# Kernel tuning notes

Measured on AMD Instinct MI355X. Metric: run time of the kernel, lower is better.

Reference implementation:

```python
import jax, jax.numpy as jnp
import numpy as np


def setup_inputs() -> dict:
    key = jax.random.key(0)
    ks = jax.random.split(key, 4)
    B, D, H, W, C = 1, 24, 24, 24, 256
    C_ = C // 8
    x = jax.random.normal(ks[0], (B, D, H, W, C), dtype=jnp.float32)
    # 1x1x1 Conv3D kernels are just [C_in, C_out] matrices (glorot-ish scale)
    wg = jax.random.normal(ks[1], (C, C_), dtype=jnp.float32) * (1.0 / np.sqrt(C))
    wf = jax.random.normal(ks[2], (C, C_), dtype=jnp.float32) * (1.0 / np.sqrt(C))
    wh = jax.random.normal(ks[3], (C, C), dtype=jnp.float32) * (1.0 / np.sqrt(C))
    bg = jnp.zeros((C_,), dtype=jnp.float32)
    bf = jnp.zeros((C_,), dtype=jnp.float32)
    bh = jnp.zeros((C,), dtype=jnp.float32)
    gamma = jnp.zeros((C,), dtype=jnp.float32)  # module initializes gamma to zeros
    return {"x": x, "wg": wg, "bg": bg, "wf": wf, "bf": bf, "wh": wh, "bh": bh, "gamma": gamma}


def reference(x, wg, bg, wf, bf, wh, bh, gamma):
    B, D, H, W, C = x.shape
    N = D * H * W
    xt = x.reshape(B, N, C)                      # [B, N, C] tokens
    x_g = jnp.einsum('bnc,cf->bnf', xt, wg) + bg  # [B, N, C_] (query)
    x_f = jnp.einsum('bnc,cf->bnf', xt, wf) + bf  # [B, N, C_] (key)
    x_h = jnp.einsum('bnc,cd->bnd', xt, wh) + bh  # [B, N, C]  (value)
    s = jnp.einsum('bnf,bmf->bnm', x_g, x_f)      # [B, N, N] scores
    s = jax.nn.softmax(s, axis=-1)
    o = jnp.einsum('bnm,bmd->bnd', s, x_h)        # [B, N, C]
    o = o.reshape(B, D, H, W, C)
    return gamma * o + x
```

## Files before the change

### kernel.cpp

```cpp
#include <hip/hip_runtime.h>
#include <math.h>

#define N_TOK 13824
#define KT 64
#define LOG2E 1.44269504088896f
#define M0 40.0f

typedef __attribute__((ext_vector_type(8)))  short bf16x8;
typedef __attribute__((ext_vector_type(4)))  float f32x4;
typedef __attribute__((ext_vector_type(16))) float f32x16;
typedef __attribute__((ext_vector_type(8)))  unsigned short u16x8;
typedef unsigned short u16;

#define AS3(p) ((__attribute__((address_space(3))) void*)(p))
#define AS1(p) ((const __attribute__((address_space(1))) void*)(p))
#define GLL(gp, lp) __builtin_amdgcn_global_load_lds(AS1(gp), AS3(lp), 16, 0, 0)

__device__ inline u16 f2b(float v) {
    union { float f; unsigned u; } a; a.f = v;
    unsigned r = a.u + 0x7fffu + ((a.u >> 16) & 1u);
    return (u16)(r >> 16);
}
__device__ inline float b2f(u16 v) {
    union { unsigned u; float f; } a; a.u = ((unsigned)v) << 16; return a.f;
}
__device__ inline float dev_exp2(float x) {
    float r;
    asm volatile("v_exp_f32 %0, %1" : "=v"(r) : "v"(x));
    return r;
}
__device__ inline float cross_sum(float v) {
    float a = v, b = v;
    asm volatile("v_permlane32_swap_b32 %0, %1" : "+v"(a), "+v"(b));
    return a + b;
}
__device__ inline unsigned cvtpk(float lo, float hi) {
    unsigned r;
    asm volatile("v_cvt_pk_bf16_f32 %0, %1, %2" : "=v"(r) : "v"(lo), "v"(hi));
    return r;
}

__global__ __launch_bounds__(512) void prep_kernel(
    const float* __restrict__ wh, const float* __restrict__ wg,
    const float* __restrict__ wf, u16* __restrict__ wt)
{
    int id = blockIdx.x * 512 + threadIdx.x;
    if (id < 320 * 256) {
        int n = id >> 8, k = id & 255;
        float v = (n < 256) ? wh[k * 256 + n]
                : (n < 288) ? wg[k * 32 + (n - 256)] * LOG2E
                            : wf[k * 32 + (n - 288)];
        wt[n * 256 + k] = f2b(v);
    }
}

__global__ __launch_bounds__(256) void proj_kernel(
    const float* __restrict__ x, const u16* __restrict__ wt,
    const float* __restrict__ bg, const float* __restrict__ bfv, const float* __restrict__ bh,
    u16* __restrict__ g, u16* __restrict__ f, u16* __restrict__ ht)
{
    __shared__ float Asf[4096];
    __shared__ u16 Bs[64 * 64];
    const int t = threadIdx.x, l = t & 63, w = t >> 6;
    const int m0 = blockIdx.x * 64, n0 = blockIdx.y * 64;
    const int mh = (w & 1) * 32, nh = (w >> 1) * 32;
    f32x4 acc[2][2] = {};

    int aoff[4];
    #pragma unroll
    for (int i = 0; i < 4; ++i) {
        int p = i * 256 + t;
        int row = p >> 4, up = p & 15, uu = up ^ (row & 15);
        aoff[i] = row * 256 + uu * 4;
    }

    for (int kstep = 0; kstep < 4; ++kstep) {
        const int k0 = kstep * 64;
        __syncthreads();
        #pragma unroll
        for (int i = 0; i < 4; ++i)
            GLL(x + (size_t)m0 * 256 + k0 + aoff[i], Asf + (i * 256 + t) * 4);
        #pragma unroll
        for (int i = 0; i < 2; ++i) {
            int ch  = w * 2 + i;
            int row = ch * 8 + (l >> 3);
            int ul  = (l & 7) ^ ((l >> 3) & 7);
            GLL(wt + (size_t)(n0 + row) * 256 + k0 + ul * 8, Bs + ch * 512);
        }
        asm volatile("s_waitcnt vmcnt(0)" ::: "memory");
        __syncthreads();
        #pragma unroll
        for (int ks = 0; ks < 2; ++ks) {
            bf16x8 a[2], b[2];
            #pragma unroll
            for (int mf = 0; mf < 2; ++mf) {
                int row = mh + mf * 16 + (l & 15);
                int uu0 = ks * 8 + (l >> 4) * 2;
                f32x4 f0 = *(const f32x4*)&Asf[(row * 16 + (uu0 ^ (row & 15))) * 4];
                f32x4 f1 = *(const f32x4*)&Asf[(row * 16 + ((uu0 + 1) ^ (row & 15))) * 4];
                union { unsigned u[4]; bf16x8 v; } av;
                av.u[0] = cvtpk(f0[0], f0[1]);
                av.u[1] = cvtpk(f0[2], f0[3]);
                av.u[2] = cvtpk(f1[0], f1[1]);
                av.u[3] = cvtpk(f1[2], f1[3]);
                a[mf] = av.v;
            }
            #pragma unroll
            for (int nf = 0; nf < 2; ++nf) {
                int row = nh + nf * 16 + (l & 15);
                int u   = (ks * 4 + (l >> 4)) ^ (row & 7);
                b[nf] = *(const bf16x8*)(Bs + row * 64 + u * 8);
            }
            #pragma unroll
            for (int mf = 0; mf < 2; ++mf)
                #pragma unroll
                for (int nf = 0; nf < 2; ++nf)
                    acc[mf][nf] = __builtin_amdgcn_mfma_f32_16x16x32_bf16(
                        a[mf], b[nf], acc[mf][nf], 0, 0, 0);
        }
    }

    #pragma unroll
    for (int mf = 0; mf < 2; ++mf)
        #pragma unroll
        for (int nf = 0; nf < 2; ++nf) {
            const int row0 = m0 + mh + mf * 16 + (l >> 4) * 4;
            const int col  = n0 + nh + nf * 16 + (l & 15);
            if (col < 256) {
                const float bias = bh[col];
                ushort4 o;
                o.x = f2b(acc[mf][nf][0] + bias);
                o.y = f2b(acc[mf][nf][1] + bias);
                o.z = f2b(acc[mf][nf][2] + bias);
                o.w = f2b(acc[mf][nf][3] + bias);
                *(ushort4*)(ht + (size_t)col * N_TOK + row0) = o;
            } else {
                const float bias = (col < 288) ? bg[col - 256] * LOG2E : bfv[col - 288];
                #pragma unroll
                for (int r = 0; r < 4; ++r) {
                    u16 v = f2b(acc[mf][nf][r] + bias);
                    if (col < 288) g[(size_t)(row0 + r) * 32 + (col - 256)] = v;
                    else           f[(size_t)(row0 + r) * 32 + (col - 288)] = v;
                }
            }
        }
}

__global__ __launch_bounds__(256, 2) void attn_kernel(
    const u16* __restrict__ g, const u16* __restrict__ fk, const u16* __restrict__ ht,
    u16* __restrict__ po, float* __restrict__ pl,
    int kps, int ntiles, int nwg)
{
    __shared__ u16 VtF[2 * 16384];
    __shared__ u16 KsF[2 * 2048];

    int orig = blockIdx.x + blockIdx.y * 108;
    int qd = nwg >> 3, rr = nwg & 7;
    int xcd = orig & 7, idx = orig >> 3;
    int wgid = (xcd < rr ? xcd * (qd + 1) : rr * (qd + 1) + (xcd - rr) * qd) + idx;
    const int split = wgid / 108;
    const int qblk  = wgid % 108;

    const int t = threadIdx.x, l = t & 63, w = t >> 6;
    const int hi = l >> 5, l31 = l & 31;
    const int q0 = qblk * 128 + w * 32;
    const int kbase = split * kps;

    bf16x8 qf0 = *(const bf16x8*)(g + (size_t)(q0 + l31) * 32 + hi * 8);
    bf16x8 qf1 = *(const bf16x8*)(g + (size_t)(q0 + l31) * 32 + 16 + hi * 8);

    f32x16 acc[8] = {};
    float l_run = 0.f;

    const u16* vbase = ht + kbase;
    int voffV[8];
    #pragma unroll
    for (int i = 0; i < 8; ++i) {
        int u = i * 256 + t;
        int ch = u >> 3, gg = u & 7, kg = gg ^ (ch & 7);
        voffV[i] = ch * N_TOK + kg * 8;
    }
    int koffK;
    { int key = t >> 2, gcu = t & 3, cu = gcu ^ ((key >> 1) & 3);
      koffK = key * 32 + cu * 8; }
    const u16* kbp = fk + (size_t)kbase * 32;

    int rbV[4];
    #pragma unroll
    for (int i = 0; i < 4; ++i) {
        int kg = i * 2 + hi;
        rbV[i] = l31 * 64 + ((kg ^ (l31 & 7)) * 8);
    }
    int rbK[2];
    #pragma unroll
    for (int ks = 0; ks < 2; ++ks)
        rbK[ks] = l31 * 4 * 8 + (((ks * 2 + hi) ^ ((l31 >> 1) & 3)) * 8);

    auto stage = [&](int tile, int db) {
        const u16* vs = vbase + tile * KT;
        #pragma unroll
        for (int i = 0; i < 8; ++i)
            GLL(vs + voffV[i], &VtF[db * 16384 + (i * 256 + t) * 8]);
        GLL(kbp + tile * (KT * 32) + koffK, &KsF[db * 2048 + t * 8]);
    };

    stage(0, 0);

    auto pvblock = [&](int b, int kb, unsigned pa[2][4]) {
        #pragma unroll
        for (int ks = 0; ks < 2; ++ks) {
            union { unsigned u[4]; bf16x8 v; } pb;
            pb.u[0] = pa[ks][0]; pb.u[1] = pa[ks][1];
            pb.u[2] = pa[ks][2]; pb.u[3] = pa[ks][3];
            #pragma unroll
            for (int cht = 0; cht < 8; ++cht) {
                bf16x8 vf = *(const bf16x8*)&VtF[b * 16384 + cht * 2048 + rbV[kb * 2 + ks]];
                acc[cht] = __builtin_amdgcn_mfma_f32_32x32x16_bf16(
                    pb.v, vf, acc[cht], 0, 0, 0);
            }
        }
    };

    auto softpa = [&](const f32x16& s, unsigned pa[2][4]) -> float {
        float pv[16];
        #pragma unroll
        for (int r = 0; r < 16; ++r) pv[r] = dev_exp2(s[r] - M0);
        #pragma unroll
        for (int ks = 0; ks < 2; ++ks) {
            const int o = ks * 8;
            unsigned a0 = cvtpk(pv[o + 0], pv[o + 1]);
            unsigned b0 = cvtpk(pv[o + 2], pv[o + 3]);
            unsigned a1 = cvtpk(pv[o + 4], pv[o + 5]);
            unsigned b1 = cvtpk(pv[o + 6], pv[o + 7]);
            asm volatile("v_permlane32_swap_b32 %0, %1" : "+v"(a0), "+v"(a1));
            asm volatile("v_permlane32_swap_b32 %0, %1" : "+v"(b0), "+v"(b1));
            pa[ks][0] = a0; pa[ks][1] = b0;
            pa[ks][2] = a1; pa[ks][3] = b1;
        }
        float s8[8];
        #pragma unroll
        for (int i = 0; i < 8; ++i) s8[i] = pv[i] + pv[i + 8];
        float s4a = s8[0] + s8[1], s4b = s8[2] + s8[3];
        float s4c = s8[4] + s8[5], s4d = s8[6] + s8[7];
        return (s4a + s4b) + (s4c + s4d);
    };

    auto sub = [&](int b, int cur) {
        asm volatile("" ::: "memory");
        __builtin_amdgcn_s_barrier();
        asm volatile("" ::: "memory");
        { int nx = cur + 1 < ntiles ? cur + 1 : 0; stage(nx, b ^ 1); }
        asm volatile("s_waitcnt vmcnt(9)" ::: "memory");
        __builtin_amdgcn_s_barrier();
        asm volatile("" ::: "memory");

        bf16x8 kf[2][2];
        #pragma unroll
        for (int kb = 0; kb < 2; ++kb)
            #pragma unroll
            for (int ks = 0; ks < 2; ++ks)
                kf[kb][ks] = *(const bf16x8*)&KsF[b * 2048 + kb * 1024 + rbK[ks]];

        f32x16 s0, s1;
        {
            f32x16 zz = {};
            zz = __builtin_amdgcn_mfma_f32_32x32x16_bf16(kf[0][0], qf0, zz, 0, 0, 0);
            s0 = __builtin_amdgcn_mfma_f32_32x32x16_bf16(kf[0][1], qf1, zz, 0, 0, 0);
        }
        {
            f32x16 zz = {};
            zz = __builtin_amdgcn_mfma_f32_32x32x16_bf16(kf[1][0], qf0, zz, 0, 0, 0);
            s1 = __builtin_amdgcn_mfma_f32_32x32x16_bf16(kf[1][1], qf1, zz, 0, 0, 0);
        }

        unsigned pa0[2][4], pa1[2][4];
        float t0 = softpa(s0, pa0);
        pvblock(b, 0, pa0);
        float t1 = softpa(s1, pa1);
        pvblock(b, 1, pa1);
        l_run += t0 + t1;
    };

    for (int tl = 0; tl < ntiles; tl += 2) {
        sub(0, tl);
        sub(1, tl + 1);
    }

    #pragma unroll
    for (int cht = 0; cht < 8; ++cht) {
        int ch = cht * 32 + l31;
        #pragma unroll
        for (int r = 0; r < 16; ++r) {
            int qq = q0 + (r & 3) + 8 * (r >> 2) + 4 * hi;
            po[((size_t)split * N_TOK + qq) * 256 + ch] = f2b(acc[cht][r]);
        }
    }
    float lfull = cross_sum(l_run);
    if (hi == 0) {
        int qq = q0 + l31;
        pl[(size_t)split * N_TOK + qq] = lfull;
    }
}

__global__ __launch_bounds__(256) void combine_kernel(
    const u16* __restrict__ po, const float* __restrict__ pl,
    const float* __restrict__ x, const float* __restrict__ gamma, float* __restrict__ out,
    int nsplit)
{
    const int t = threadIdx.x;
    const int q = blockIdx.x * 8 + (t >> 5);
    const int c8 = (t & 31) * 8;

    float lsum = 0.f, o[8] = {};
    for (int s = 0; s < nsplit; ++s) {
        lsum += pl[(size_t)s * N_TOK + q];
        u16x8 p8 = *(const u16x8*)(po + ((size_t)s * N_TOK + q) * 256 + c8);
        #pragma unroll
        for (int j = 0; j < 8; ++j) o[j] += b2f(p8[j]);
    }
    float inv = 1.f / lsum;
    float4 gm0 = *(const float4*)(gamma + c8);
    float4 gm1 = *(const float4*)(gamma + c8 + 4);
    float4 xv0 = *(const float4*)(x + (size_t)q * 256 + c8);
    float4 xv1 = *(const float4*)(x + (size_t)q * 256 + c8 + 4);
    float4 ov0, ov1;
    ov0.x = gm0.x * (o[0] * inv) + xv0.x;
    ov0.y = gm0.y * (o[1] * inv) + xv0.y;
    ov0.z = gm0.z * (o[2] * inv) + xv0.z;
    ov0.w = gm0.w * (o[3] * inv) + xv0.w;
    ov1.x = gm1.x * (o[4] * inv) + xv1.x;
    ov1.y = gm1.y * (o[5] * inv) + xv1.y;
    ov1.z = gm1.z * (o[6] * inv) + xv1.z;
    ov1.w = gm1.w * (o[7] * inv) + xv1.w;
    *(float4*)(out + (size_t)q * 256 + c8)     = ov0;
    *(float4*)(out + (size_t)q * 256 + c8 + 4) = ov1;
}

extern "C" void kernel_launch(void* const* d_in, const int* in_sizes, int n_in,
                              void* d_out, int out_size, void* d_ws, size_t ws_size,
                              hipStream_t stream) {
    const float* x     = (const float*)d_in[0];
    const float* wg    = (const float*)d_in[1];
    const float* bg    = (const float*)d_in[2];
    const float* wf    = (const float*)d_in[3];
    const float* bfv   = (const float*)d_in[4];
    const float* wh    = (const float*)d_in[5];
    const float* bh    = (const float*)d_in[6];
    const float* gamma = (const float*)d_in[7];
    float* out = (float*)d_out;

    const size_t base_b = (size_t)N_TOK * 640;
    auto need = [&](int ns) {
        return base_b + (size_t)ns * N_TOK * 512 + (size_t)ns * N_TOK * 8
             + 320 * 256 * 2 + 1024;
    };
    int nsplit = 4;
    if (ws_size >= need(9)) nsplit = 9;
    else if (ws_size >= need(6)) nsplit = 6;
    const int kps = N_TOK / nsplit, ntiles = kps / KT;
    const int nwg = 108 * nsplit;

    u16* ws = (u16*)d_ws;
    u16* gq = ws;
    u16* fk = gq + (size_t)N_TOK * 32;
    u16* ht = fk + (size_t)N_TOK * 32;
    u16* po = ht + (size_t)N_TOK * 256;
    u16* wt = po + (size_t)nsplit * N_TOK * 256;
    float* pl = (float*)(wt + 320 * 256);

    prep_kernel<<<160, 512, 0, stream>>>(wh, wg, wf, wt);
    proj_kernel<<<dim3(216, 5), 256, 0, stream>>>(x, wt, bg, bfv, bh, gq, fk, ht);
    attn_kernel<<<dim3(108, nsplit), 256, 0, stream>>>(gq, fk, ht, po, pl, kps, ntiles, nwg);
    combine_kernel<<<N_TOK / 8, 256, 0, stream>>>(po, pl, x, gamma, out, nsplit);
}
```

Before: 143.6 us.

## Shrink attention workgroups to two waves with 32-key tiles and new LDS swizzle

The attention kernel now uses 128-thread workgroups, each covering 64 queries instead of 128, with key tiles of 32 instead of 64. The launch grid doubles to 216 blocks per split, and the LDS staging layout and swizzle are rewritten to match the smaller tiles. Each iteration now does one score block instead of two. The aim is more, smaller workgroups, which should fill the CUs better and cut per-block LDS use. The cost is that each loaded V/K tile is reused by fewer queries and there are twice as many barrier and stage rounds per key.

```diff
diff --git a/kernel.cpp b/kernel.cpp
--- a/kernel.cpp
+++ b/kernel.cpp
@@ -2,7 +2,7 @@
 #include <math.h>
 
 #define N_TOK 13824
-#define KT 64
+#define KT 32
 #define LOG2E 1.44269504088896f
 #define M0 40.0f
 
@@ -146,24 +146,24 @@
         }
 }
 
-__global__ __launch_bounds__(256, 2) void attn_kernel(
+__global__ __launch_bounds__(128, 2) void attn_kernel(
     const u16* __restrict__ g, const u16* __restrict__ fk, const u16* __restrict__ ht,
     u16* __restrict__ po, float* __restrict__ pl,
     int kps, int ntiles, int nwg)
 {
-    __shared__ u16 VtF[2 * 16384];
-    __shared__ u16 KsF[2 * 2048];
-
-    int orig = blockIdx.x + blockIdx.y * 108;
+    __shared__ u16 VtF[2 * 8192];
+    __shared__ u16 KsF[2 * 1024];
+
+    int orig = blockIdx.x + blockIdx.y * 216;
     int qd = nwg >> 3, rr = nwg & 7;
     int xcd = orig & 7, idx = orig >> 3;
     int wgid = (xcd < rr ? xcd * (qd + 1) : rr * (qd + 1) + (xcd - rr) * qd) + idx;
-    const int split = wgid / 108;
-    const int qblk  = wgid % 108;
+    const int split = wgid / 216;
+    const int qblk  = wgid % 216;
 
     const int t = threadIdx.x, l = t & 63, w = t >> 6;
     const int hi = l >> 5, l31 = l & 31;
-    const int q0 = qblk * 128 + w * 32;
+    const int q0 = qblk * 64 + w * 32;
     const int kbase = split * kps;
 
     bf16x8 qf0 = *(const bf16x8*)(g + (size_t)(q0 + l31) * 32 + hi * 8);
@@ -176,55 +176,58 @@
     int voffV[8];
     #pragma unroll
     for (int i = 0; i < 8; ++i) {
-        int u = i * 256 + t;
-        int ch = u >> 3, gg = u & 7, kg = gg ^ (ch & 7);
+        int u = i * 128 + t;
+        int row = u >> 3, inp = (u & 7) ^ (row & 7);
+        int ch = row * 2 + (inp >> 2), kg = inp & 3;
         voffV[i] = ch * N_TOK + kg * 8;
     }
     int koffK;
-    { int key = t >> 2, gcu = t & 3, cu = gcu ^ ((key >> 1) & 3);
-      koffK = key * 32 + cu * 8; }
+    {
+        int row = t >> 3, inp = (t & 7) ^ (row & 7);
+        int key = row * 2 + (inp >> 2), cu = inp & 3;
+        koffK = key * 32 + cu * 8;
+    }
     const u16* kbp = fk + (size_t)kbase * 32;
 
-    int rbV[4];
-    #pragma unroll
-    for (int i = 0; i < 4; ++i) {
-        int kg = i * 2 + hi;
-        rbV[i] = l31 * 64 + ((kg ^ (l31 & 7)) * 8);
-    }
-    int rbK[2];
-    #pragma unroll
-    for (int ks = 0; ks < 2; ++ks)
-        rbK[ks] = l31 * 4 * 8 + (((ks * 2 + hi) ^ ((l31 >> 1) & 3)) * 8);
+    const int r2 = l31 >> 1, lo1 = (l31 & 1) * 4;
+    int rbV[2], rbK[2];
+    #pragma unroll
+    for (int ks = 0; ks < 2; ++ks) {
+        int inner = lo1 + ks * 2 + hi;
+        rbV[ks] = (r2 * 8 + (inner ^ (r2 & 7))) * 8;
+        rbK[ks] = (r2 * 8 + (inner ^ (r2 & 7))) * 8;
+    }
 
     auto stage = [&](int tile, int db) {
         const u16* vs = vbase + tile * KT;
         #pragma unroll
         for (int i = 0; i < 8; ++i)
-            GLL(vs + voffV[i], &VtF[db * 16384 + (i * 256 + t) * 8]);
-        GLL(kbp + tile * (KT * 32) + koffK, &KsF[db * 2048 + t * 8]);
+            GLL(vs + voffV[i], &VtF[db * 8192 + (i * 128 + t) * 8]);
+        GLL(kbp + tile * (KT * 32) + koffK, &KsF[db * 1024 + t * 8]);
     };
 
     stage(0, 0);
 
-    auto pvblock = [&](int b, int kb, unsigned pa[2][4]) {
-        #pragma unroll
-        for (int ks = 0; ks < 2; ++ks) {
-            union { unsigned u[4]; bf16x8 v; } pb;
-            pb.u[0] = pa[ks][0]; pb.u[1] = pa[ks][1];
-            pb.u[2] = pa[ks][2]; pb.u[3] = pa[ks][3];
-            #pragma unroll
-            for (int cht = 0; cht < 8; ++cht) {
-                bf16x8 vf = *(const bf16x8*)&VtF[b * 16384 + cht * 2048 + rbV[kb * 2 + ks]];
-                acc[cht] = __builtin_amdgcn_mfma_f32_32x32x16_bf16(
-                    pb.v, vf, acc[cht], 0, 0, 0);
-            }
-        }
-    };
-
-    auto softpa = [&](const f32x16& s, unsigned pa[2][4]) -> float {
+    auto sub = [&](int b, int cur) {
+        asm volatile("" ::: "memory");
+        __builtin_amdgcn_s_barrier();
+        asm volatile("" ::: "memory");
+        { int nx = cur + 1 < ntiles ? cur + 1 : 0; stage(nx, b ^ 1); }
+        asm volatile("s_waitcnt vmcnt(9)" ::: "memory");
+        __builtin_amdgcn_s_barrier();
+        asm volatile("" ::: "memory");
+
+        bf16x8 kf0 = *(const bf16x8*)&KsF[b * 1024 + rbK[0]];
+        bf16x8 kf1 = *(const bf16x8*)&KsF[b * 1024 + rbK[1]];
+
+        f32x16 zz = {};
+        zz = __builtin_amdgcn_mfma_f32_32x32x16_bf16(kf0, qf0, zz, 0, 0, 0);
+        f32x16 s = __builtin_amdgcn_mfma_f32_32x32x16_bf16(kf1, qf1, zz, 0, 0, 0);
+
         float pv[16];
         #pragma unroll
         for (int r = 0; r < 16; ++r) pv[r] = dev_exp2(s[r] - M0);
+        unsigned pa[2][4];
         #pragma unroll
         for (int ks = 0; ks < 2; ++ks) {
             const int o = ks * 8;
@@ -237,48 +240,26 @@
             pa[ks][0] = a0; pa[ks][1] = b0;
             pa[ks][2] = a1; pa[ks][3] = b1;
         }
+
+        #pragma unroll
+        for (int ks = 0; ks < 2; ++ks) {
+            union { unsigned u[4]; bf16x8 v; } pb;
+            pb.u[0] = pa[ks][0]; pb.u[1] = pa[ks][1];
+            pb.u[2] = pa[ks][2]; pb.u[3] = pa[ks][3];
+            #pragma unroll
+            for (int cht = 0; cht < 8; ++cht) {
+                bf16x8 vf = *(const bf16x8*)&VtF[b * 8192 + cht * 1024 + rbV[ks]];
+                acc[cht] = __builtin_amdgcn_mfma_f32_32x32x16_bf16(
+                    pb.v, vf, acc[cht], 0, 0, 0);
+            }
+        }
+
         float s8[8];
         #pragma unroll
         for (int i = 0; i < 8; ++i) s8[i] = pv[i] + pv[i + 8];
         float s4a = s8[0] + s8[1], s4b = s8[2] + s8[3];
         float s4c = s8[4] + s8[5], s4d = s8[6] + s8[7];
-        return (s4a + s4b) + (s4c + s4d);
-    };
-
-    auto sub = [&](int b, int cur) {
-        asm volatile("" ::: "memory");
-        __builtin_amdgcn_s_barrier();
-        asm volatile("" ::: "memory");
-        { int nx = cur + 1 < ntiles ? cur + 1 : 0; stage(nx, b ^ 1); }
-        asm volatile("s_waitcnt vmcnt(9)" ::: "memory");
-        __builtin_amdgcn_s_barrier();
-        asm volatile("" ::: "memory");
-
-        bf16x8 kf[2][2];
-        #pragma unroll
-        for (int kb = 0; kb < 2; ++kb)
-            #pragma unroll
-            for (int ks = 0; ks < 2; ++ks)
-                kf[kb][ks] = *(const bf16x8*)&KsF[b * 2048 + kb * 1024 + rbK[ks]];
-
-        f32x16 s0, s1;
-        {
-            f32x16 zz = {};
-            zz = __builtin_amdgcn_mfma_f32_32x32x16_bf16(kf[0][0], qf0, zz, 0, 0, 0);
-            s0 = __builtin_amdgcn_mfma_f32_32x32x16_bf16(kf[0][1], qf1, zz, 0, 0, 0);
-        }
-        {
-            f32x16 zz = {};
-            zz = __builtin_amdgcn_mfma_f32_32x32x16_bf16(kf[1][0], qf0, zz, 0, 0, 0);
-            s1 = __builtin_amdgcn_mfma_f32_32x32x16_bf16(kf[1][1], qf1, zz, 0, 0, 0);
-        }
-
-        unsigned pa0[2][4], pa1[2][4];
-        float t0 = softpa(s0, pa0);
-        pvblock(b, 0, pa0);
-        float t1 = softpa(s1, pa1);
-        pvblock(b, 1, pa1);
-        l_run += t0 + t1;
+        l_run += (s4a + s4b) + (s4c + s4d);
     };
 
     for (int tl = 0; tl < ntiles; tl += 2) {
@@ -358,7 +339,7 @@
     if (ws_size >= need(9)) nsplit = 9;
     else if (ws_size >= need(6)) nsplit = 6;
     const int kps = N_TOK / nsplit, ntiles = kps / KT;
-    const int nwg = 108 * nsplit;
+    const int nwg = 216 * nsplit;
 
     u16* ws = (u16*)d_ws;
     u16* gq = ws;
@@ -370,6 +351,6 @@
 
     prep_kernel<<<160, 512, 0, stream>>>(wh, wg, wf, wt);
     proj_kernel<<<dim3(216, 5), 256, 0, stream>>>(x, wt, bg, bfv, bh, gq, fk, ht);
-    attn_kernel<<<dim3(108, nsplit), 256, 0, stream>>>(gq, fk, ht, po, pl, kps, ntiles, nwg);
+    attn_kernel<<<dim3(216, nsplit), 128, 0, stream>>>(gq, fk, ht, po, pl, kps, ntiles, nwg);
     combine_kernel<<<N_TOK / 8, 256, 0, stream>>>(po, pl, x, gamma, out, nsplit);
 }
```

Result: slower. 169.5 us (+18.1%).
